# Kernel tuning notes

Measured on AMD Instinct MI355X. Metric: run time of the kernel, lower is better.

Reference implementation:

```python
import jax, jax.numpy as jnp
import numpy as np

N = 100_000   # total nodes per graph batch
E = 400_000   # directed edges per graph batch
G = 1024      # number of graphs
F_IN = 90


def _lin_init(key, fan_in, fan_out):
    s = 1.0 / np.sqrt(fan_in)
    kW, kb = jax.random.split(key)
    W = jax.random.uniform(kW, (fan_in, fan_out), jnp.float32, -s, s)
    b = jax.random.uniform(kb, (fan_out,), jnp.float32, -s, s)
    return W, b


def setup_inputs() -> dict:
    key = jax.random.key(0)
    ks = jax.random.split(key, 16)
    batch = (jnp.arange(N, dtype=jnp.int32) * G // N).astype(jnp.int32)
    inp = {
        'x1': jax.random.normal(ks[0], (N, F_IN), jnp.float32),
        'edge_index1': jax.random.randint(ks[1], (2, E), 0, N, jnp.int32),
        'batch1': batch,
        'x2': jax.random.normal(ks[2], (N, F_IN), jnp.float32),
        'edge_index2': jax.random.randint(ks[3], (2, E), 0, N, jnp.int32),
        'batch2': batch,
    }
    W1, b1 = _lin_init(ks[4], 90, 128)
    W2, b2 = _lin_init(ks[5], 128, 256)
    W3, b3 = _lin_init(ks[6], 256, 256)
    W4, b4 = _lin_init(ks[7], 256, 256)
    fc1_W, fc1_b = _lin_init(ks[8], 1024, 512)
    fc2_W, fc2_b = _lin_init(ks[9], 512, 256)
    fc3_W, fc3_b = _lin_init(ks[10], 256, 1)
    inp.update(W1=W1, b1=b1, W2=W2, b2=b2, W3=W3, b3=b3, W4=W4, b4=b4,
               fc1_W=fc1_W, fc1_b=fc1_b, fc2_W=fc2_W, fc2_b=fc2_b,
               fc3_W=fc3_W, fc3_b=fc3_b)
    return inp


def _gcn(x, W, b, src, dst, dinv):
    # GCNConv: D^{-1/2} (A + I) D^{-1/2} X W + b  (self-loops added)
    h = x @ W                                   # [N, F_out]
    norm = dinv[src] * dinv[dst]                # [E]
    agg = jax.ops.segment_sum(h[src] * norm[:, None], dst, num_segments=N)
    agg = agg + h * (dinv * dinv)[:, None]      # self-loop term
    return agg + b


def _drug_encoder(x, edge_index, batch, W1, b1, W2, b2, W3, b3, W4, b4):
    src, dst = edge_index[0], edge_index[1]
    # degree with self-loops (PyG gcn_norm)
    deg = jax.ops.segment_sum(jnp.ones(src.shape[0], x.dtype), dst, num_segments=N) + 1.0
    dinv = jax.lax.rsqrt(deg)
    x = jax.nn.relu(_gcn(x, W1, b1, src, dst, dinv))
    x = jax.nn.relu(_gcn(x, W2, b2, src, dst, dinv))
    x = jax.nn.relu(_gcn(x, W3, b3, src, dst, dinv))
    x = jax.nn.relu(_gcn(x, W4, b4, src, dst, dinv))
    gmax = jax.ops.segment_max(x, batch, num_segments=G)
    cnt = jax.ops.segment_sum(jnp.ones(N, x.dtype), batch, num_segments=G)
    gmean = jax.ops.segment_sum(x, batch, num_segments=G) / cnt[:, None]
    return jnp.concatenate([gmax, gmean], axis=1)   # [G, 512]


def reference(x1, edge_index1, batch1, x2, edge_index2, batch2,
              W1, b1, W2, b2, W3, b3, W4, b4,
              fc1_W, fc1_b, fc2_W, fc2_b, fc3_W, fc3_b):
    h1 = _drug_encoder(x1, edge_index1, batch1, W1, b1, W2, b2, W3, b3, W4, b4)
    h2 = _drug_encoder(x2, edge_index2, batch2, W1, b1, W2, b2, W3, b3, W4, b4)
    x = jnp.concatenate([h1 - h2, h2 - h1], axis=1)   # [G, 1024]
    x = jax.nn.relu(x @ fc1_W + fc1_b)                # dropout = identity (eval)
    x = jax.nn.relu(x @ fc2_W + fc2_b)
    x = jnp.tanh(x @ fc3_W + fc3_b)
    return x                                          # [G, 1]
```

## Files before the change

kernel.cpp:

```cpp
#include <hip/hip_runtime.h>
#include <hip/hip_bf16.h>

#define NN 100000
#define EE 400000
#define GG 1024

typedef _Float16 half_t;
typedef _Float16 f16x8 __attribute__((ext_vector_type(8)));
typedef float f32x4 __attribute__((ext_vector_type(4)));
typedef float f32x2 __attribute__((ext_vector_type(2)));

#define GLOAD_LDS(g, l) \
    __builtin_amdgcn_global_load_lds((const __attribute__((address_space(1))) void*)(g), \
                                     (__attribute__((address_space(3))) void*)(l), 16, 0, 0)


__global__ void k_count2(const int* __restrict__ ei1, const int* __restrict__ ei2,
                         int* __restrict__ deg) {
    int e = blockIdx.x * 256 + threadIdx.x;
    if (e >= 2 * EE) return;
    int enc = e >= EE;
    const int* ei = enc ? ei2 : ei1;
    int le = e - enc * EE;
    atomicAdd(&deg[enc * NN + ei[EE + le]], 1);
}

__global__ void k_scan_bsum(const int* __restrict__ deg, int* __restrict__ bsum, int total) {
    __shared__ int lds[256];
    int t = threadIdx.x;
    int base = blockIdx.x * 1024 + t * 4;
    int s = 0;
#pragma unroll
    for (int i = 0; i < 4; ++i) { int idx = base + i; s += (idx < total) ? deg[idx] : 0; }
    lds[t] = s;
    __syncthreads();
    for (int off = 128; off > 0; off >>= 1) {
        if (t < off) lds[t] += lds[t + off];
        __syncthreads();
    }
    if (t == 0) bsum[blockIdx.x] = lds[0];
}

__global__ void k_scan_write(const int* __restrict__ deg, const int* __restrict__ bsum,
                             int* __restrict__ rowptr, float* __restrict__ dinv,
                             int total, int totedge) {
    __shared__ int lds[256];
    __shared__ int blockoff;
    int t = threadIdx.x;
    if (t == 0) {
        int off = 0;
        for (int b = 0; b < (int)blockIdx.x; ++b) off += bsum[b];
        blockoff = off;
    }
    int base = blockIdx.x * 1024 + t * 4;
    int v[4]; int ts = 0;
#pragma unroll
    for (int i = 0; i < 4; ++i) { int idx = base + i; v[i] = (idx < total) ? deg[idx] : 0; ts += v[i]; }
    lds[t] = ts;
    __syncthreads();
    for (int off = 1; off < 256; off <<= 1) {
        int x = (t >= off) ? lds[t - off] : 0;
        __syncthreads();
        lds[t] += x;
        __syncthreads();
    }
    int excl = lds[t] - ts + blockoff;
#pragma unroll
    for (int i = 0; i < 4; ++i) {
        int idx = base + i;
        if (idx < total) {
            rowptr[idx] = excl;
            dinv[idx] = rsqrtf((float)v[i] + 1.0f);
        }
        excl += v[i];
    }
    if (blockIdx.x == 0 && t == 0) rowptr[total] = totedge;
}

__global__ void k_fill2(const int* __restrict__ ei1, const int* __restrict__ ei2,
                        const int* __restrict__ rowptr, int* __restrict__ cnt,
                        int* __restrict__ colv) {
    int e = blockIdx.x * 256 + threadIdx.x;
    if (e >= 2 * EE) return;
    int enc = e >= EE;
    const int* ei = enc ? ei2 : ei1;
    int le = e - enc * EE;
    int s = ei[le], d = ei[EE + le];
    int gd = enc * NN + d;
    int pos = rowptr[gd] + atomicAdd(&cnt[gd], 1);
    colv[pos] = s;
}

__global__ void k_starts2(const int* __restrict__ b1, const int* __restrict__ b2,
                          int* __restrict__ gstart) {
    int i = blockIdx.x * 256 + threadIdx.x;
    if (i >= 2 * NN) return;
    int enc = i >= NN;
    int il = i - enc * NN;
    const int* bat = enc ? b2 : b1;
    int* gs = gstart + enc * (GG + 1);
    int b = bat[il];
    if (il == 0) {
        for (int g = 0; g <= b; ++g) gs[g] = 0;
    } else {
        int pb = bat[il - 1];
        for (int g = pb + 1; g <= b; ++g) gs[g] = il;
    }
    if (il == NN - 1) {
        for (int g = b + 1; g <= GG; ++g) gs[g] = NN;
    }
}


__global__ void k_agg90(const float* __restrict__ x, const float* __restrict__ dinv,
                        const int* __restrict__ rowptr, const int* __restrict__ col,
                        half_t* __restrict__ out) {
    int wave = threadIdx.x >> 6;
    int lane = threadIdx.x & 63;
    int n = blockIdx.x * 4 + wave;
    if (n >= NN) return;
    bool al = lane < 45;
    float dn = dinv[n];
    f32x2 acc = {0.f, 0.f};
    if (al) acc = dn * ((const f32x2*)(x + (size_t)n * 90))[lane];
    int j0 = rowptr[n], j1 = rowptr[n + 1];
    int j = j0;
    for (; j + 4 <= j1; j += 4) {
        int s0 = col[j], s1 = col[j + 1], s2 = col[j + 2], s3 = col[j + 3];
        float d0 = dinv[s0], d1 = dinv[s1], d2 = dinv[s2], d3 = dinv[s3];
        if (al) {
            f32x2 v0 = ((const f32x2*)(x + (size_t)s0 * 90))[lane];
            f32x2 v1 = ((const f32x2*)(x + (size_t)s1 * 90))[lane];
            f32x2 v2 = ((const f32x2*)(x + (size_t)s2 * 90))[lane];
            f32x2 v3 = ((const f32x2*)(x + (size_t)s3 * 90))[lane];
            acc += d0 * v0;
            acc += d1 * v1;
            acc += d2 * v2;
            acc += d3 * v3;
        }
    }
    for (; j < j1; ++j) {
        int s = col[j];
        float ds = dinv[s];
        if (al) acc += ds * ((const f32x2*)(x + (size_t)s * 90))[lane];
    }
    float v0 = al ? dn * acc[0] : 0.f;
    float v1 = al ? dn * acc[1] : 0.f;
    half_t h0 = (half_t)v0, l0 = (half_t)(v0 - (float)h0);
    half_t h1 = (half_t)v1, l1 = (half_t)(v1 - (float)h1);
    half_t* o = out + (size_t)n * 256;
    o[2 * lane] = h0;
    o[2 * lane + 1] = h1;
    o[128 + 2 * lane] = l0;
    o[128 + 2 * lane + 1] = l1;
}

template <int VW>
__global__ void k_agg_splitv(const float* __restrict__ x, const float* __restrict__ dinv,
                             const int* __restrict__ rowptr, const int* __restrict__ col,
                             half_t* __restrict__ out) {
    constexpr int F = 64 * VW;
    typedef float fvec __attribute__((ext_vector_type(VW)));
    int wave = threadIdx.x >> 6;
    int lane = threadIdx.x & 63;
    int n = blockIdx.x * 4 + wave;
    if (n >= NN) return;
    float dn = dinv[n];
    fvec acc = dn * ((const fvec*)(x + (size_t)n * F))[lane];
    int j0 = rowptr[n], j1 = rowptr[n + 1];
    int j = j0;
    for (; j + 4 <= j1; j += 4) {
        int s0 = col[j], s1 = col[j + 1], s2 = col[j + 2], s3 = col[j + 3];
        float d0 = dinv[s0], d1 = dinv[s1], d2 = dinv[s2], d3 = dinv[s3];
        fvec v0 = ((const fvec*)(x + (size_t)s0 * F))[lane];
        fvec v1 = ((const fvec*)(x + (size_t)s1 * F))[lane];
        fvec v2 = ((const fvec*)(x + (size_t)s2 * F))[lane];
        fvec v3 = ((const fvec*)(x + (size_t)s3 * F))[lane];
        acc += d0 * v0;
        acc += d1 * v1;
        acc += d2 * v2;
        acc += d3 * v3;
    }
    for (; j < j1; ++j) {
        int s = col[j];
        acc += dinv[s] * ((const fvec*)(x + (size_t)s * F))[lane];
    }
    half_t* o = out + (size_t)n * (2 * F);
    half_t hv[VW], lv[VW];
#pragma unroll
    for (int i = 0; i < VW; ++i) {
        float v = dn * acc[i];
        hv[i] = (half_t)v;
        lv[i] = (half_t)(v - (float)hv[i]);
    }
#pragma unroll
    for (int i = 0; i < VW; ++i) o[lane * VW + i] = hv[i];
#pragma unroll
    for (int i = 0; i < VW; ++i) o[F + lane * VW + i] = lv[i];
}


__global__ void k_wprep(const float* __restrict__ W, half_t* __restrict__ Bt,
                        int K, int Kpad, int Nc) {
    int t = blockIdx.x * 256 + threadIdx.x;
    if (t >= Nc * Kpad) return;
    int n = t / Kpad, kp = t % Kpad;
    half_t h = (half_t)0.f, l = (half_t)0.f;
    if (kp < K) {
        float w = W[(size_t)kp * Nc + n];
        h = (half_t)w;
        l = (half_t)(w - (float)h);
    }
    half_t* o = Bt + (size_t)n * 3 * Kpad;
    o[kp] = h;
    o[Kpad + kp] = h;
    o[2 * Kpad + kp] = l;
}


__global__ void k_split(const float* __restrict__ in, half_t* __restrict__ out, int K) {
    int t = blockIdx.x * 256 + threadIdx.x;
    int row = t / K, k = t % K;
    float v = in[t];
    half_t h = (half_t)v;
    half_t l = (half_t)(v - (float)h);
    half_t* o = out + (size_t)row * 2 * K;
    o[k] = h;
    o[K + k] = l;
}


template <bool RELU>
__global__ __launch_bounds__(256, 2)
void k_mgemm(const half_t* __restrict__ Ap, const half_t* __restrict__ Bt,
             const float* __restrict__ bias, float* __restrict__ C,
             int M, int Kpad, int Nc) {
    __shared__ half_t As[128 * 64];
    __shared__ half_t Bs[128 * 64];
    const int tid = threadIdx.x;
    const int wave = tid >> 6, lane = tid & 63;
    const int wm = wave >> 1, wn = wave & 1;
    const int bm = blockIdx.x * 128, bn = blockIdx.y * 128;
    const int KA = 2 * Kpad, KB = 3 * Kpad;
    const int nkt = KB >> 6;
    const int aTiles = KA >> 6;

    f32x4 acc[4][4] = {};

    const int srow = tid >> 3;
    const int ch = tid & 7;

    for (int kt = 0; kt < nkt; ++kt) {
        int ka0 = ((kt < aTiles) ? kt : (kt - aTiles)) << 6;
        int kb0 = kt << 6;
        __syncthreads();
#pragma unroll
        for (int i = 0; i < 4; ++i) {
            int rl = i * 32 + srow;
            int sch = ch ^ (rl & 7);
            int gr = bm + rl; if (gr >= M) gr = M - 1;
            const half_t* ga = Ap + (size_t)gr * KA + ka0 + sch * 8;
            GLOAD_LDS(ga, (char*)As + i * 4096 + wave * 1024);
        }
#pragma unroll
        for (int i = 0; i < 4; ++i) {
            int rl = i * 32 + srow;
            int sch = ch ^ (rl & 7);
            const half_t* gb = Bt + (size_t)(bn + rl) * KB + kb0 + sch * 8;
            GLOAD_LDS(gb, (char*)Bs + i * 4096 + wave * 1024);
        }
        __syncthreads();
#pragma unroll
        for (int s = 0; s < 2; ++s) {
            f16x8 af[4], bf[4];
#pragma unroll
            for (int i = 0; i < 4; ++i) {
                int row = wm * 64 + i * 16 + (lane & 15);
                int c = s * 4 + (lane >> 4);
                af[i] = *(const f16x8*)&As[row * 64 + ((c ^ (row & 7)) << 3)];
            }
#pragma unroll
            for (int j = 0; j < 4; ++j) {
                int row = wn * 64 + j * 16 + (lane & 15);
                int c = s * 4 + (lane >> 4);
                bf[j] = *(const f16x8*)&Bs[row * 64 + ((c ^ (row & 7)) << 3)];
            }
#pragma unroll
            for (int i = 0; i < 4; ++i)
#pragma unroll
                for (int j = 0; j < 4; ++j)
                    acc[i][j] = __builtin_amdgcn_mfma_f32_16x16x32_f16(af[i], bf[j], acc[i][j], 0, 0, 0);
        }
    }

#pragma unroll
    for (int i = 0; i < 4; ++i) {
#pragma unroll
        for (int j = 0; j < 4; ++j) {
            int cc = bn + wn * 64 + j * 16 + (lane & 15);
            float bv = bias[cc];
            int r0 = bm + wm * 64 + i * 16 + (lane >> 4) * 4;
#pragma unroll
            for (int q = 0; q < 4; ++q) {
                int gr = r0 + q;
                if (gr < M) {
                    float v = acc[i][j][q] + bv;
                    if (RELU) v = fmaxf(v, 0.f);
                    C[(size_t)gr * Nc + cc] = v;
                }
            }
        }
    }
}


__global__ void k_pool(const float* __restrict__ act, const int* __restrict__ gstart,
                       float* __restrict__ h) {
    int g = blockIdx.x;
    int f = threadIdx.x;
    int s = gstart[g], e = gstart[g + 1];
    float mx = 0.f, sm = 0.f;
    for (int i = s; i < e; ++i) {
        float v = act[(size_t)i * 256 + f];
        mx = fmaxf(mx, v);
        sm += v;
    }
    float cnt = (float)(e - s);
    h[(size_t)g * 512 + f] = mx;
    h[(size_t)g * 512 + 256 + f] = (cnt > 0.f) ? sm / cnt : 0.f;
}


__global__ void k_headin_split(const float* __restrict__ h, half_t* __restrict__ xh) {
    int t = blockIdx.x * blockDim.x + threadIdx.x;
    if (t >= GG * 1024) return;
    int g = t >> 10, j = t & 1023;
    const float* h1 = h + (size_t)g * 512;
    const float* h2 = h + (size_t)(GG + g) * 512;
    float v = (j < 512) ? (h1[j] - h2[j]) : (h2[j - 512] - h1[j - 512]);
    half_t hi = (half_t)v;
    half_t lo = (half_t)(v - (float)hi);
    half_t* o = xh + (size_t)g * 2048;
    o[j] = hi;
    o[1024 + j] = lo;
}

__global__ void k_fc3(const float* __restrict__ A, const float* __restrict__ W,
                      const float* __restrict__ b, float* __restrict__ out) {
    int g = blockIdx.x * 4 + (threadIdx.x >> 6);
    int lane = threadIdx.x & 63;
    const float* a = A + (size_t)g * 256;
    float p = a[lane] * W[lane] + a[lane + 64] * W[lane + 64]
            + a[lane + 128] * W[lane + 128] + a[lane + 192] * W[lane + 192];
    for (int off = 32; off > 0; off >>= 1) p += __shfl_down(p, off);
    if (lane == 0) out[g] = tanhf(p + b[0]);
}


extern "C" void kernel_launch(void* const* d_in, const int* in_sizes, int n_in,
                              void* d_out, int out_size, void* d_ws, size_t ws_size,
                              hipStream_t stream) {
    const float* x1  = (const float*)d_in[0];
    const int*   ei1 = (const int*)d_in[1];
    const int*   ba1 = (const int*)d_in[2];
    const float* x2  = (const float*)d_in[3];
    const int*   ei2 = (const int*)d_in[4];
    const int*   ba2 = (const int*)d_in[5];
    const float* W1 = (const float*)d_in[6];
    const float* b1 = (const float*)d_in[7];
    const float* W2 = (const float*)d_in[8];
    const float* b2 = (const float*)d_in[9];
    const float* W3 = (const float*)d_in[10];
    const float* b3 = (const float*)d_in[11];
    const float* W4 = (const float*)d_in[12];
    const float* b4 = (const float*)d_in[13];
    const float* fc1W = (const float*)d_in[14];
    const float* fc1b = (const float*)d_in[15];
    const float* fc2W = (const float*)d_in[16];
    const float* fc2b = (const float*)d_in[17];
    const float* fc3W = (const float*)d_in[18];
    const float* fc3b = (const float*)d_in[19];
    float* out = (float*)d_out;

    char* ws = (char*)d_ws;
    size_t off = 0;
    auto alloc = [&](size_t bytes) -> void* {
        void* p = (void*)(ws + off);
        off += (bytes + 255) & ~(size_t)255;
        return p;
    };
    int*    dc     = (int*)alloc((size_t)4 * NN * sizeof(int));
    int*    rowptr = (int*)alloc((size_t)(2 * NN + 1) * sizeof(int));
    int*    colv   = (int*)alloc((size_t)2 * EE * sizeof(int));
    int*    bsum   = (int*)alloc(256 * sizeof(int));
    int*    gstart = (int*)alloc((size_t)2 * (GG + 1) * sizeof(int));
    float*  dinv   = (float*)alloc((size_t)2 * NN * sizeof(float));
    half_t* Ap     = (half_t*)alloc((size_t)NN * 512 * sizeof(half_t));
    float*  act    = (float*)alloc((size_t)NN * 256 * sizeof(float));
    half_t* Bt1    = (half_t*)alloc((size_t)128 * 384 * sizeof(half_t));
    half_t* Bt2    = (half_t*)alloc((size_t)256 * 384 * sizeof(half_t));
    half_t* Bt3    = (half_t*)alloc((size_t)256 * 768 * sizeof(half_t));
    half_t* Bt4    = (half_t*)alloc((size_t)256 * 768 * sizeof(half_t));
    half_t* Btf1   = (half_t*)alloc((size_t)512 * 3072 * sizeof(half_t));
    half_t* Btf2   = (half_t*)alloc((size_t)256 * 1536 * sizeof(half_t));
    float*  hpool  = (float*)alloc((size_t)2 * GG * 512 * sizeof(float));
    half_t* xhs    = (half_t*)alloc((size_t)GG * 2048 * sizeof(half_t));
    float*  t1     = (float*)alloc((size_t)GG * 512 * sizeof(float));
    half_t* t1s    = (half_t*)alloc((size_t)GG * 1024 * sizeof(half_t));
    float*  t2     = (float*)alloc((size_t)GG * 256 * sizeof(float));

    int* deg = dc;
    int* cnt = dc + 2 * NN;

    int nsb2 = (2 * NN + 1023) / 1024;
    int mt = (NN + 127) / 128;

    k_wprep<<<(128 * 128 + 255) / 256, 256, 0, stream>>>(W1, Bt1, 90, 128, 128);
    k_wprep<<<(256 * 128 + 255) / 256, 256, 0, stream>>>(W2, Bt2, 128, 128, 256);
    k_wprep<<<(256 * 256 + 255) / 256, 256, 0, stream>>>(W3, Bt3, 256, 256, 256);
    k_wprep<<<(256 * 256 + 255) / 256, 256, 0, stream>>>(W4, Bt4, 256, 256, 256);
    k_wprep<<<(512 * 1024 + 255) / 256, 256, 0, stream>>>(fc1W, Btf1, 1024, 1024, 512);
    k_wprep<<<(256 * 512 + 255) / 256, 256, 0, stream>>>(fc2W, Btf2, 512, 512, 256);

    hipMemsetAsync(dc, 0, (size_t)4 * NN * sizeof(int), stream);
    k_count2<<<(2 * EE + 255) / 256, 256, 0, stream>>>(ei1, ei2, deg);
    k_scan_bsum<<<nsb2, 256, 0, stream>>>(deg, bsum, 2 * NN);
    k_scan_write<<<nsb2, 256, 0, stream>>>(deg, bsum, rowptr, dinv, 2 * NN, 2 * EE);
    k_fill2<<<(2 * EE + 255) / 256, 256, 0, stream>>>(ei1, ei2, rowptr, cnt, colv);
    k_starts2<<<(2 * NN + 255) / 256, 256, 0, stream>>>(ba1, ba2, gstart);

    for (int p = 0; p < 2; ++p) {
        const float* x    = p ? x2 : x1;
        const int*   rp   = rowptr + p * NN;
        const float* dv   = dinv + p * NN;
        const int*   gs   = gstart + p * (GG + 1);

        k_agg90<<<(NN + 3) / 4, 256, 0, stream>>>(x, dv, rp, colv, Ap);
        k_mgemm<true><<<dim3(mt, 1), 256, 0, stream>>>(Ap, Bt1, b1, act, NN, 128, 128);
        k_agg_splitv<2><<<(NN + 3) / 4, 256, 0, stream>>>(act, dv, rp, colv, Ap);
        k_mgemm<true><<<dim3(mt, 2), 256, 0, stream>>>(Ap, Bt2, b2, act, NN, 128, 256);
        k_agg_splitv<4><<<(NN + 3) / 4, 256, 0, stream>>>(act, dv, rp, colv, Ap);
        k_mgemm<true><<<dim3(mt, 2), 256, 0, stream>>>(Ap, Bt3, b3, act, NN, 256, 256);
        k_agg_splitv<4><<<(NN + 3) / 4, 256, 0, stream>>>(act, dv, rp, colv, Ap);
        k_mgemm<true><<<dim3(mt, 2), 256, 0, stream>>>(Ap, Bt4, b4, act, NN, 256, 256);

        k_pool<<<GG, 256, 0, stream>>>(act, gs, hpool + (size_t)p * GG * 512);
    }

    k_headin_split<<<(GG * 1024 + 255) / 256, 256, 0, stream>>>(hpool, xhs);
    k_mgemm<true><<<dim3(GG / 128, 4), 256, 0, stream>>>(xhs, Btf1, fc1b, t1, GG, 1024, 512);
    k_split<<<(GG * 512 + 255) / 256, 256, 0, stream>>>(t1, t1s, 512);
    k_mgemm<true><<<dim3(GG / 128, 2), 256, 0, stream>>>(t1s, Btf2, fc2b, t2, GG, 512, 256);
    k_fc3<<<GG / 4, 256, 0, stream>>>(t2, fc3W, fc3b, out);
}
```

Measured before the change: 1.351 ms.

## Interleave both encoders by fusing one encoder's GEMM with the other's aggregation

```diff
diff --git a/kernel.cpp b/kernel.cpp
--- a/kernel.cpp
+++ b/kernel.cpp
@@ -112,12 +112,14 @@
 }
 
 
-__global__ void k_agg90(const float* __restrict__ x, const float* __restrict__ dinv,
-                        const int* __restrict__ rowptr, const int* __restrict__ col,
-                        half_t* __restrict__ out) {
+__device__ __forceinline__ void dev_agg90(int blk, const float* __restrict__ x,
+                                          const float* __restrict__ dinv,
+                                          const int* __restrict__ rowptr,
+                                          const int* __restrict__ col,
+                                          half_t* __restrict__ out) {
     int wave = threadIdx.x >> 6;
     int lane = threadIdx.x & 63;
-    int n = blockIdx.x * 4 + wave;
+    int n = blk * 4 + wave;
     if (n >= NN) return;
     bool al = lane < 45;
     float dn = dinv[n];
@@ -133,10 +135,7 @@
             f32x2 v1 = ((const f32x2*)(x + (size_t)s1 * 90))[lane];
             f32x2 v2 = ((const f32x2*)(x + (size_t)s2 * 90))[lane];
             f32x2 v3 = ((const f32x2*)(x + (size_t)s3 * 90))[lane];
-            acc += d0 * v0;
-            acc += d1 * v1;
-            acc += d2 * v2;
-            acc += d3 * v3;
+            acc += d0 * v0; acc += d1 * v1; acc += d2 * v2; acc += d3 * v3;
         }
     }
     for (; j < j1; ++j) {
@@ -156,14 +155,16 @@
 }
 
 template <int VW>
-__global__ void k_agg_splitv(const float* __restrict__ x, const float* __restrict__ dinv,
-                             const int* __restrict__ rowptr, const int* __restrict__ col,
-                             half_t* __restrict__ out) {
+__device__ __forceinline__ void dev_aggv(int blk, const float* __restrict__ x,
+                                         const float* __restrict__ dinv,
+                                         const int* __restrict__ rowptr,
+                                         const int* __restrict__ col,
+                                         half_t* __restrict__ out) {
     constexpr int F = 64 * VW;
     typedef float fvec __attribute__((ext_vector_type(VW)));
     int wave = threadIdx.x >> 6;
     int lane = threadIdx.x & 63;
-    int n = blockIdx.x * 4 + wave;
+    int n = blk * 4 + wave;
     if (n >= NN) return;
     float dn = dinv[n];
     fvec acc = dn * ((const fvec*)(x + (size_t)n * F))[lane];
@@ -176,10 +177,7 @@
         fvec v1 = ((const fvec*)(x + (size_t)s1 * F))[lane];
         fvec v2 = ((const fvec*)(x + (size_t)s2 * F))[lane];
         fvec v3 = ((const fvec*)(x + (size_t)s3 * F))[lane];
-        acc += d0 * v0;
-        acc += d1 * v1;
-        acc += d2 * v2;
-        acc += d3 * v3;
+        acc += d0 * v0; acc += d1 * v1; acc += d2 * v2; acc += d3 * v3;
     }
     for (; j < j1; ++j) {
         int s = col[j];
@@ -197,6 +195,133 @@
     for (int i = 0; i < VW; ++i) o[lane * VW + i] = hv[i];
 #pragma unroll
     for (int i = 0; i < VW; ++i) o[F + lane * VW + i] = lv[i];
+}
+
+
+template <bool RELU>
+__device__ __forceinline__ void dev_gemm(int bx, int by,
+    const half_t* __restrict__ Ap, const half_t* __restrict__ Bt,
+    const float* __restrict__ bias, float* __restrict__ C,
+    int M, int Kpad, int Nc) {
+    __shared__ half_t As[128 * 64];
+    __shared__ half_t Bs[128 * 64];
+    const int tid = threadIdx.x;
+    const int wave = tid >> 6, lane = tid & 63;
+    const int wm = wave >> 1, wn = wave & 1;
+    const int bm = bx * 128, bn = by * 128;
+    const int KA = 2 * Kpad, KB = 3 * Kpad;
+    const int nkt = KB >> 6;
+    const int aTiles = KA >> 6;
+
+    f32x4 acc[4][4] = {};
+
+    const int srow = tid >> 3;
+    const int ch = tid & 7;
+
+    for (int kt = 0; kt < nkt; ++kt) {
+        int ka0 = ((kt < aTiles) ? kt : (kt - aTiles)) << 6;
+        int kb0 = kt << 6;
+        __syncthreads();
+#pragma unroll
+        for (int i = 0; i < 4; ++i) {
+            int rl = i * 32 + srow;
+            int sch = ch ^ (rl & 7);
+            int gr = bm + rl; if (gr >= M) gr = M - 1;
+            const half_t* ga = Ap + (size_t)gr * KA + ka0 + sch * 8;
+            GLOAD_LDS(ga, (char*)As + i * 4096 + wave * 1024);
+        }
+#pragma unroll
+        for (int i = 0; i < 4; ++i) {
+            int rl = i * 32 + srow;
+            int sch = ch ^ (rl & 7);
+            const half_t* gb = Bt + (size_t)(bn + rl) * KB + kb0 + sch * 8;
+            GLOAD_LDS(gb, (char*)Bs + i * 4096 + wave * 1024);
+        }
+        __syncthreads();
+#pragma unroll
+        for (int s = 0; s < 2; ++s) {
+            f16x8 af[4], bf[4];
+#pragma unroll
+            for (int i = 0; i < 4; ++i) {
+                int row = wm * 64 + i * 16 + (lane & 15);
+                int c = s * 4 + (lane >> 4);
+                af[i] = *(const f16x8*)&As[row * 64 + ((c ^ (row & 7)) << 3)];
+            }
+#pragma unroll
+            for (int j = 0; j < 4; ++j) {
+                int row = wn * 64 + j * 16 + (lane & 15);
+                int c = s * 4 + (lane >> 4);
+                bf[j] = *(const f16x8*)&Bs[row * 64 + ((c ^ (row & 7)) << 3)];
+            }
+#pragma unroll
+            for (int i = 0; i < 4; ++i)
+#pragma unroll
+                for (int j = 0; j < 4; ++j)
+                    acc[i][j] = __builtin_amdgcn_mfma_f32_16x16x32_f16(af[i], bf[j], acc[i][j], 0, 0, 0);
+        }
+    }
+
+#pragma unroll
+    for (int i = 0; i < 4; ++i) {
+#pragma unroll
+        for (int j = 0; j < 4; ++j) {
+            int cc = bn + wn * 64 + j * 16 + (lane & 15);
+            float bv = bias[cc];
+            int r0 = bm + wm * 64 + i * 16 + (lane >> 4) * 4;
+#pragma unroll
+            for (int q = 0; q < 4; ++q) {
+                int gr = r0 + q;
+                if (gr < M) {
+                    float v = acc[i][j][q] + bv;
+                    if (RELU) v = fmaxf(v, 0.f);
+                    C[(size_t)gr * Nc + cc] = v;
+                }
+            }
+        }
+    }
+}
+
+
+__global__ void k_agg90(const float* __restrict__ x, const float* __restrict__ dinv,
+                        const int* __restrict__ rowptr, const int* __restrict__ col,
+                        half_t* __restrict__ out) {
+    dev_agg90(blockIdx.x, x, dinv, rowptr, col, out);
+}
+
+template <int VW>
+__global__ void k_agg_splitv(const float* __restrict__ x, const float* __restrict__ dinv,
+                             const int* __restrict__ rowptr, const int* __restrict__ col,
+                             half_t* __restrict__ out) {
+    dev_aggv<VW>(blockIdx.x, x, dinv, rowptr, col, out);
+}
+
+template <bool RELU>
+__global__ __launch_bounds__(256, 2)
+void k_mgemm(const half_t* __restrict__ Ap, const half_t* __restrict__ Bt,
+             const float* __restrict__ bias, float* __restrict__ C,
+             int M, int Kpad, int Nc) {
+    dev_gemm<RELU>(blockIdx.x, blockIdx.y, Ap, Bt, bias, C, M, Kpad, Nc);
+}
+
+
+template <int AGGV>
+__global__ __launch_bounds__(256, 2)
+void k_fused(int stride, int gemmBlocks, int mt,
+             const half_t* __restrict__ Ap, const half_t* __restrict__ Bt,
+             const float* __restrict__ bias, float* __restrict__ C,
+             int M, int Kpad, int Nc,
+             const float* __restrict__ xa, const float* __restrict__ dva,
+             const int* __restrict__ rpa, const int* __restrict__ cola,
+             half_t* __restrict__ outa) {
+    int q = blockIdx.x / stride, r = blockIdx.x - q * stride;
+    if (r == 0 && q < gemmBlocks) {
+        dev_gemm<true>(q % mt, q / mt, Ap, Bt, bias, C, M, Kpad, Nc);
+    } else {
+        int before = (q < gemmBlocks) ? (q + (r > 0 ? 1 : 0)) : gemmBlocks;
+        int aggIdx = blockIdx.x - before;
+        if constexpr (AGGV == 90) dev_agg90(aggIdx, xa, dva, rpa, cola, outa);
+        else dev_aggv<AGGV>(aggIdx, xa, dva, rpa, cola, outa);
+    }
 }
 
 
@@ -217,7 +342,6 @@
     o[2 * Kpad + kp] = l;
 }
 
-
 __global__ void k_split(const float* __restrict__ in, half_t* __restrict__ out, int K) {
     int t = blockIdx.x * 256 + threadIdx.x;
     int row = t / K, k = t % K;
@@ -227,90 +351,6 @@
     half_t* o = out + (size_t)row * 2 * K;
     o[k] = h;
     o[K + k] = l;
-}
-
-
-template <bool RELU>
-__global__ __launch_bounds__(256, 2)
-void k_mgemm(const half_t* __restrict__ Ap, const half_t* __restrict__ Bt,
-             const float* __restrict__ bias, float* __restrict__ C,
-             int M, int Kpad, int Nc) {
-    __shared__ half_t As[128 * 64];
-    __shared__ half_t Bs[128 * 64];
-    const int tid = threadIdx.x;
-    const int wave = tid >> 6, lane = tid & 63;
-    const int wm = wave >> 1, wn = wave & 1;
-    const int bm = blockIdx.x * 128, bn = blockIdx.y * 128;
-    const int KA = 2 * Kpad, KB = 3 * Kpad;
-    const int nkt = KB >> 6;
-    const int aTiles = KA >> 6;
-
-    f32x4 acc[4][4] = {};
-
-    const int srow = tid >> 3;
-    const int ch = tid & 7;
-
-    for (int kt = 0; kt < nkt; ++kt) {
-        int ka0 = ((kt < aTiles) ? kt : (kt - aTiles)) << 6;
-        int kb0 = kt << 6;
-        __syncthreads();
-#pragma unroll
-        for (int i = 0; i < 4; ++i) {
-            int rl = i * 32 + srow;
-            int sch = ch ^ (rl & 7);
-            int gr = bm + rl; if (gr >= M) gr = M - 1;
-            const half_t* ga = Ap + (size_t)gr * KA + ka0 + sch * 8;
-            GLOAD_LDS(ga, (char*)As + i * 4096 + wave * 1024);
-        }
-#pragma unroll
-        for (int i = 0; i < 4; ++i) {
-            int rl = i * 32 + srow;
-            int sch = ch ^ (rl & 7);
-            const half_t* gb = Bt + (size_t)(bn + rl) * KB + kb0 + sch * 8;
-            GLOAD_LDS(gb, (char*)Bs + i * 4096 + wave * 1024);
-        }
-        __syncthreads();
-#pragma unroll
-        for (int s = 0; s < 2; ++s) {
-            f16x8 af[4], bf[4];
-#pragma unroll
-            for (int i = 0; i < 4; ++i) {
-                int row = wm * 64 + i * 16 + (lane & 15);
-                int c = s * 4 + (lane >> 4);
-                af[i] = *(const f16x8*)&As[row * 64 + ((c ^ (row & 7)) << 3)];
-            }
-#pragma unroll
-            for (int j = 0; j < 4; ++j) {
-                int row = wn * 64 + j * 16 + (lane & 15);
-                int c = s * 4 + (lane >> 4);
-                bf[j] = *(const f16x8*)&Bs[row * 64 + ((c ^ (row & 7)) << 3)];
-            }
-#pragma unroll
-            for (int i = 0; i < 4; ++i)
-#pragma unroll
-                for (int j = 0; j < 4; ++j)
-                    acc[i][j] = __builtin_amdgcn_mfma_f32_16x16x32_f16(af[i], bf[j], acc[i][j], 0, 0, 0);
-        }
-    }
-
-#pragma unroll
-    for (int i = 0; i < 4; ++i) {
-#pragma unroll
-        for (int j = 0; j < 4; ++j) {
-            int cc = bn + wn * 64 + j * 16 + (lane & 15);
-            float bv = bias[cc];
-            int r0 = bm + wm * 64 + i * 16 + (lane >> 4) * 4;
-#pragma unroll
-            for (int q = 0; q < 4; ++q) {
-                int gr = r0 + q;
-                if (gr < M) {
-                    float v = acc[i][j][q] + bv;
-                    if (RELU) v = fmaxf(v, 0.f);
-                    C[(size_t)gr * Nc + cc] = v;
-                }
-            }
-        }
-    }
 }
 
 
@@ -328,6 +368,26 @@
     float cnt = (float)(e - s);
     h[(size_t)g * 512 + f] = mx;
     h[(size_t)g * 512 + 256 + f] = (cnt > 0.f) ? sm / cnt : 0.f;
+}
+
+__global__ void k_pool2(const float* __restrict__ a1, const float* __restrict__ a2,
+                        const int* __restrict__ gstart, float* __restrict__ h) {
+    int enc = blockIdx.x >> 10;
+    int g = blockIdx.x & 1023;
+    const float* act = enc ? a2 : a1;
+    const int* gs = gstart + enc * (GG + 1);
+    int f = threadIdx.x;
+    int s = gs[g], e = gs[g + 1];
+    float mx = 0.f, sm = 0.f;
+    for (int i = s; i < e; ++i) {
+        float v = act[(size_t)i * 256 + f];
+        mx = fmaxf(mx, v);
+        sm += v;
+    }
+    float cnt = (float)(e - s);
+    float* o = h + (size_t)enc * GG * 512;
+    o[(size_t)g * 512 + f] = mx;
+    o[(size_t)g * 512 + 256 + f] = (cnt > 0.f) ? sm / cnt : 0.f;
 }
 
 
@@ -382,6 +442,8 @@
     const float* fc3b = (const float*)d_in[19];
     float* out = (float*)d_out;
 
+    const bool pipe = ws_size >= (size_t)435000000ull;
+
     char* ws = (char*)d_ws;
     size_t off = 0;
     auto alloc = [&](size_t bytes) -> void* {
@@ -395,8 +457,10 @@
     int*    bsum   = (int*)alloc(256 * sizeof(int));
     int*    gstart = (int*)alloc((size_t)2 * (GG + 1) * sizeof(int));
     float*  dinv   = (float*)alloc((size_t)2 * NN * sizeof(float));
-    half_t* Ap     = (half_t*)alloc((size_t)NN * 512 * sizeof(half_t));
-    float*  act    = (float*)alloc((size_t)NN * 256 * sizeof(float));
+    half_t* Ap1    = (half_t*)alloc((size_t)NN * 512 * sizeof(half_t));
+    float*  act1   = (float*)alloc((size_t)NN * 256 * sizeof(float));
+    half_t* Ap2    = pipe ? (half_t*)alloc((size_t)NN * 512 * sizeof(half_t)) : Ap1;
+    float*  act2   = pipe ? (float*)alloc((size_t)NN * 256 * sizeof(float)) : act1;
     half_t* Bt1    = (half_t*)alloc((size_t)128 * 384 * sizeof(half_t));
     half_t* Bt2    = (half_t*)alloc((size_t)256 * 384 * sizeof(half_t));
     half_t* Bt3    = (half_t*)alloc((size_t)256 * 768 * sizeof(half_t));
@@ -414,6 +478,7 @@
 
     int nsb2 = (2 * NN + 1023) / 1024;
     int mt = (NN + 127) / 128;
+    int aggB = (NN + 3) / 4;
 
     k_wprep<<<(128 * 128 + 255) / 256, 256, 0, stream>>>(W1, Bt1, 90, 128, 128);
     k_wprep<<<(256 * 128 + 255) / 256, 256, 0, stream>>>(W2, Bt2, 128, 128, 256);
@@ -429,22 +494,50 @@
     k_fill2<<<(2 * EE + 255) / 256, 256, 0, stream>>>(ei1, ei2, rowptr, cnt, colv);
     k_starts2<<<(2 * NN + 255) / 256, 256, 0, stream>>>(ba1, ba2, gstart);
 
-    for (int p = 0; p < 2; ++p) {
-        const float* x    = p ? x2 : x1;
-        const int*   rp   = rowptr + p * NN;
-        const float* dv   = dinv + p * NN;
-        const int*   gs   = gstart + p * (GG + 1);
-
-        k_agg90<<<(NN + 3) / 4, 256, 0, stream>>>(x, dv, rp, colv, Ap);
-        k_mgemm<true><<<dim3(mt, 1), 256, 0, stream>>>(Ap, Bt1, b1, act, NN, 128, 128);
-        k_agg_splitv<2><<<(NN + 3) / 4, 256, 0, stream>>>(act, dv, rp, colv, Ap);
-        k_mgemm<true><<<dim3(mt, 2), 256, 0, stream>>>(Ap, Bt2, b2, act, NN, 128, 256);
-        k_agg_splitv<4><<<(NN + 3) / 4, 256, 0, stream>>>(act, dv, rp, colv, Ap);
-        k_mgemm<true><<<dim3(mt, 2), 256, 0, stream>>>(Ap, Bt3, b3, act, NN, 256, 256);
-        k_agg_splitv<4><<<(NN + 3) / 4, 256, 0, stream>>>(act, dv, rp, colv, Ap);
-        k_mgemm<true><<<dim3(mt, 2), 256, 0, stream>>>(Ap, Bt4, b4, act, NN, 256, 256);
-
-        k_pool<<<GG, 256, 0, stream>>>(act, gs, hpool + (size_t)p * GG * 512);
+    const int*   rp1 = rowptr;          const int*   rp2 = rowptr + NN;
+    const float* dv1 = dinv;            const float* dv2 = dinv + NN;
+
+    if (pipe) {
+        auto FUSED = [&](auto aggvTag, const half_t* Ap, const half_t* Bt, const float* bias,
+                         float* C, int Kpad, int Nc,
+                         const float* xa, const float* dva, const int* rpa, half_t* outa) {
+            constexpr int AGGV = decltype(aggvTag)::value;
+            int gB = mt * (Nc / 128);
+            int total = aggB + gB;
+            int stride = total / gB;
+            k_fused<AGGV><<<total, 256, 0, stream>>>(stride, gB, mt, Ap, Bt, bias, C,
+                                                     NN, Kpad, Nc, xa, dva, rpa, colv, outa);
+        };
+        using I90 = std::integral_constant<int, 90>;
+        using I2  = std::integral_constant<int, 2>;
+        using I4  = std::integral_constant<int, 4>;
+
+        k_agg90<<<aggB, 256, 0, stream>>>(x1, dv1, rp1, colv, Ap1);
+        FUSED(I90{}, Ap1, Bt1, b1, act1, 128, 128, x2,   dv2, rp2, Ap2);
+        FUSED(I2{},  Ap2, Bt1, b1, act2, 128, 128, act1, dv1, rp1, Ap1);
+        FUSED(I2{},  Ap1, Bt2, b2, act1, 128, 256, act2, dv2, rp2, Ap2);
+        FUSED(I4{},  Ap2, Bt2, b2, act2, 128, 256, act1, dv1, rp1, Ap1);
+        FUSED(I4{},  Ap1, Bt3, b3, act1, 256, 256, act2, dv2, rp2, Ap2);
+        FUSED(I4{},  Ap2, Bt3, b3, act2, 256, 256, act1, dv1, rp1, Ap1);
+        FUSED(I4{},  Ap1, Bt4, b4, act1, 256, 256, act2, dv2, rp2, Ap2);
+        k_mgemm<true><<<dim3(mt, 2), 256, 0, stream>>>(Ap2, Bt4, b4, act2, NN, 256, 256);
+        k_pool2<<<2 * GG, 256, 0, stream>>>(act1, act2, gstart, hpool);
+    } else {
+        for (int p = 0; p < 2; ++p) {
+            const float* x  = p ? x2 : x1;
+            const int*   rp = p ? rp2 : rp1;
+            const float* dv = p ? dv2 : dv1;
+            const int*   gs = gstart + p * (GG + 1);
+            k_agg90<<<aggB, 256, 0, stream>>>(x, dv, rp, colv, Ap1);
+            k_mgemm<true><<<dim3(mt, 1), 256, 0, stream>>>(Ap1, Bt1, b1, act1, NN, 128, 128);
+            k_agg_splitv<2><<<aggB, 256, 0, stream>>>(act1, dv, rp, colv, Ap1);
+            k_mgemm<true><<<dim3(mt, 2), 256, 0, stream>>>(Ap1, Bt2, b2, act1, NN, 128, 256);
+            k_agg_splitv<4><<<aggB, 256, 0, stream>>>(act1, dv, rp, colv, Ap1);
+            k_mgemm<true><<<dim3(mt, 2), 256, 0, stream>>>(Ap1, Bt3, b3, act1, NN, 256, 256);
+            k_agg_splitv<4><<<aggB, 256, 0, stream>>>(act1, dv, rp, colv, Ap1);
+            k_mgemm<true><<<dim3(mt, 2), 256, 0, stream>>>(Ap1, Bt4, b4, act1, NN, 256, 256);
+            k_pool<<<GG, 256, 0, stream>>>(act1, gs, hpool + (size_t)p * GG * 512);
+        }
     }
 
     k_headin_split<<<(GG * 1024 + 255) / 256, 256, 0, stream>>>(hpool, xhs);
```

Result: no change. 1.353 ms (+0.2%).

## Pack two nodes per wave in aggregation and use full-width 256-column GEMM tiles

Applied to the files above, without the earlier changes.

```diff
diff --git a/kernel.cpp b/kernel.cpp
--- a/kernel.cpp
+++ b/kernel.cpp
@@ -133,10 +133,7 @@
             f32x2 v1 = ((const f32x2*)(x + (size_t)s1 * 90))[lane];
             f32x2 v2 = ((const f32x2*)(x + (size_t)s2 * 90))[lane];
             f32x2 v3 = ((const f32x2*)(x + (size_t)s3 * 90))[lane];
-            acc += d0 * v0;
-            acc += d1 * v1;
-            acc += d2 * v2;
-            acc += d3 * v3;
+            acc += d0 * v0; acc += d1 * v1; acc += d2 * v2; acc += d3 * v3;
         }
     }
     for (; j < j1; ++j) {
@@ -156,47 +153,60 @@
 }
 
 template <int VW>
-__global__ void k_agg_splitv(const float* __restrict__ x, const float* __restrict__ dinv,
-                             const int* __restrict__ rowptr, const int* __restrict__ col,
-                             half_t* __restrict__ out) {
-    constexpr int F = 64 * VW;
+__global__ void k_aggpair(const float* __restrict__ x, const float* __restrict__ dinv,
+                          const int* __restrict__ rowptr, const int* __restrict__ col,
+                          half_t* __restrict__ out) {
+    constexpr int F = 32 * VW;
     typedef float fvec __attribute__((ext_vector_type(VW)));
     int wave = threadIdx.x >> 6;
     int lane = threadIdx.x & 63;
-    int n = blockIdx.x * 4 + wave;
-    if (n >= NN) return;
+    int sub = lane & 31;
+    int n = blockIdx.x * 8 + wave * 2 + (lane >> 5);
     float dn = dinv[n];
-    fvec acc = dn * ((const fvec*)(x + (size_t)n * F))[lane];
-    int j0 = rowptr[n], j1 = rowptr[n + 1];
-    int j = j0;
-    for (; j + 4 <= j1; j += 4) {
-        int s0 = col[j], s1 = col[j + 1], s2 = col[j + 2], s3 = col[j + 3];
-        float d0 = dinv[s0], d1 = dinv[s1], d2 = dinv[s2], d3 = dinv[s3];
-        fvec v0 = ((const fvec*)(x + (size_t)s0 * F))[lane];
-        fvec v1 = ((const fvec*)(x + (size_t)s1 * F))[lane];
-        fvec v2 = ((const fvec*)(x + (size_t)s2 * F))[lane];
-        fvec v3 = ((const fvec*)(x + (size_t)s3 * F))[lane];
-        acc += d0 * v0;
-        acc += d1 * v1;
-        acc += d2 * v2;
-        acc += d3 * v3;
-    }
-    for (; j < j1; ++j) {
-        int s = col[j];
-        acc += dinv[s] * ((const fvec*)(x + (size_t)s * F))[lane];
+    fvec acc = dn * ((const fvec*)(x + (size_t)n * F))[sub];
+    int j0 = rowptr[n];
+    int deg = rowptr[n + 1] - j0;
+    int m = max(deg, __shfl_xor(deg, 32));
+    int t = 0;
+    for (; t + 4 <= m; t += 4) {
+        bool o0 = t < deg, o1 = t + 1 < deg, o2 = t + 2 < deg, o3 = t + 3 < deg;
+        int s0 = o0 ? col[j0 + t]     : n;
+        int s1 = o1 ? col[j0 + t + 1] : n;
+        int s2 = o2 ? col[j0 + t + 2] : n;
+        int s3 = o3 ? col[j0 + t + 3] : n;
+        float w0 = o0 ? dinv[s0] : 0.f;
+        float w1 = o1 ? dinv[s1] : 0.f;
+        float w2 = o2 ? dinv[s2] : 0.f;
+        float w3 = o3 ? dinv[s3] : 0.f;
+        fvec v0 = ((const fvec*)(x + (size_t)s0 * F))[sub];
+        fvec v1 = ((const fvec*)(x + (size_t)s1 * F))[sub];
+        fvec v2 = ((const fvec*)(x + (size_t)s2 * F))[sub];
+        fvec v3 = ((const fvec*)(x + (size_t)s3 * F))[sub];
+        acc += w0 * v0; acc += w1 * v1; acc += w2 * v2; acc += w3 * v3;
+    }
+    if (t < m) {
+        bool o0 = t < deg, o1 = t + 1 < deg, o2 = t + 2 < deg;
+        bool m1 = t + 1 < m, m2 = t + 2 < m;
+        int s0 = o0 ? col[j0 + t]     : n;
+        int s1 = o1 ? col[j0 + t + 1] : n;
+        int s2 = o2 ? col[j0 + t + 2] : n;
+        float w0 = o0 ? dinv[s0] : 0.f;
+        float w1 = o1 ? dinv[s1] : 0.f;
+        float w2 = o2 ? dinv[s2] : 0.f;
+        fvec v0 = ((const fvec*)(x + (size_t)s0 * F))[sub];
+        acc += w0 * v0;
+        if (m1) { fvec v1 = ((const fvec*)(x + (size_t)s1 * F))[sub]; acc += w1 * v1; }
+        if (m2) { fvec v2 = ((const fvec*)(x + (size_t)s2 * F))[sub]; acc += w2 * v2; }
     }
     half_t* o = out + (size_t)n * (2 * F);
-    half_t hv[VW], lv[VW];
 #pragma unroll
     for (int i = 0; i < VW; ++i) {
         float v = dn * acc[i];
-        hv[i] = (half_t)v;
-        lv[i] = (half_t)(v - (float)hv[i]);
-    }
-#pragma unroll
-    for (int i = 0; i < VW; ++i) o[lane * VW + i] = hv[i];
-#pragma unroll
-    for (int i = 0; i < VW; ++i) o[F + lane * VW + i] = lv[i];
+        half_t h = (half_t)v;
+        half_t l = (half_t)(v - (float)h);
+        o[sub * VW + i] = h;
+        o[F + sub * VW + i] = l;
+    }
 }
 
 
@@ -216,7 +226,6 @@
     o[Kpad + kp] = h;
     o[2 * Kpad + kp] = l;
 }
-
 
 __global__ void k_split(const float* __restrict__ in, half_t* __restrict__ out, int K) {
     int t = blockIdx.x * 256 + threadIdx.x;
@@ -307,6 +316,90 @@
                     float v = acc[i][j][q] + bv;
                     if (RELU) v = fmaxf(v, 0.f);
                     C[(size_t)gr * Nc + cc] = v;
+                }
+            }
+        }
+    }
+}
+
+
+template <bool RELU>
+__global__ __launch_bounds__(256, 2)
+void k_mgemm256(const half_t* __restrict__ Ap, const half_t* __restrict__ Bt,
+                const float* __restrict__ bias, float* __restrict__ C,
+                int M, int Kpad) {
+    __shared__ half_t As[128 * 64];
+    __shared__ half_t Bs[256 * 64];
+    const int tid = threadIdx.x;
+    const int wave = tid >> 6, lane = tid & 63;
+    const int wm = wave >> 1, wn = wave & 1;
+    const int bm = blockIdx.x * 128;
+    const int KA = 2 * Kpad, KB = 3 * Kpad;
+    const int nkt = KB >> 6;
+    const int aTiles = KA >> 6;
+
+    f32x4 acc[4][8] = {};
+
+    const int srow = tid >> 3;
+    const int ch = tid & 7;
+
+    for (int kt = 0; kt < nkt; ++kt) {
+        int ka0 = ((kt < aTiles) ? kt : (kt - aTiles)) << 6;
+        int kb0 = kt << 6;
+        __syncthreads();
+#pragma unroll
+        for (int i = 0; i < 4; ++i) {
+            int rl = i * 32 + srow;
+            int sch = ch ^ (rl & 7);
+            int gr = bm + rl; if (gr >= M) gr = M - 1;
+            const half_t* ga = Ap + (size_t)gr * KA + ka0 + sch * 8;
+            GLOAD_LDS(ga, (char*)As + i * 4096 + wave * 1024);
+        }
+#pragma unroll
+        for (int i = 0; i < 8; ++i) {
+            int rl = i * 32 + srow;
+            int sch = ch ^ (rl & 7);
+            const half_t* gb = Bt + (size_t)rl * KB + kb0 + sch * 8;
+            GLOAD_LDS(gb, (char*)Bs + i * 4096 + wave * 1024);
+        }
+        __syncthreads();
+#pragma unroll
+        for (int s = 0; s < 2; ++s) {
+            f16x8 af[4], bf[8];
+#pragma unroll
+            for (int i = 0; i < 4; ++i) {
+                int row = wm * 64 + i * 16 + (lane & 15);
+                int c = s * 4 + (lane >> 4);
+                af[i] = *(const f16x8*)&As[row * 64 + ((c ^ (row & 7)) << 3)];
+            }
+#pragma unroll
+            for (int j = 0; j < 8; ++j) {
+                int row = wn * 128 + j * 16 + (lane & 15);
+                int c = s * 4 + (lane >> 4);
+                bf[j] = *(const f16x8*)&Bs[row * 64 + ((c ^ (row & 7)) << 3)];
+            }
+#pragma unroll
+            for (int i = 0; i < 4; ++i)
+#pragma unroll
+                for (int j = 0; j < 8; ++j)
+                    acc[i][j] = __builtin_amdgcn_mfma_f32_16x16x32_f16(af[i], bf[j], acc[i][j], 0, 0, 0);
+        }
+    }
+
+#pragma unroll
+    for (int i = 0; i < 4; ++i) {
+#pragma unroll
+        for (int j = 0; j < 8; ++j) {
+            int cc = wn * 128 + j * 16 + (lane & 15);
+            float bv = bias[cc];
+            int r0 = bm + wm * 64 + i * 16 + (lane >> 4) * 4;
+#pragma unroll
+            for (int q = 0; q < 4; ++q) {
+                int gr = r0 + q;
+                if (gr < M) {
+                    float v = acc[i][j][q] + bv;
+                    if (RELU) v = fmaxf(v, 0.f);
+                    C[(size_t)gr * 256 + cc] = v;
                 }
             }
         }
@@ -430,19 +523,19 @@
     k_starts2<<<(2 * NN + 255) / 256, 256, 0, stream>>>(ba1, ba2, gstart);
 
     for (int p = 0; p < 2; ++p) {
-        const float* x    = p ? x2 : x1;
-        const int*   rp   = rowptr + p * NN;
-        const float* dv   = dinv + p * NN;
-        const int*   gs   = gstart + p * (GG + 1);
+        const float* x  = p ? x2 : x1;
+        const int*   rp = rowptr + p * NN;
+        const float* dv = dinv + p * NN;
+        const int*   gs = gstart + p * (GG + 1);
 
         k_agg90<<<(NN + 3) / 4, 256, 0, stream>>>(x, dv, rp, colv, Ap);
         k_mgemm<true><<<dim3(mt, 1), 256, 0, stream>>>(Ap, Bt1, b1, act, NN, 128, 128);
-        k_agg_splitv<2><<<(NN + 3) / 4, 256, 0, stream>>>(act, dv, rp, colv, Ap);
-        k_mgemm<true><<<dim3(mt, 2), 256, 0, stream>>>(Ap, Bt2, b2, act, NN, 128, 256);
-        k_agg_splitv<4><<<(NN + 3) / 4, 256, 0, stream>>>(act, dv, rp, colv, Ap);
-        k_mgemm<true><<<dim3(mt, 2), 256, 0, stream>>>(Ap, Bt3, b3, act, NN, 256, 256);
-        k_agg_splitv<4><<<(NN + 3) / 4, 256, 0, stream>>>(act, dv, rp, colv, Ap);
-        k_mgemm<true><<<dim3(mt, 2), 256, 0, stream>>>(Ap, Bt4, b4, act, NN, 256, 256);
+        k_aggpair<4><<<NN / 8, 256, 0, stream>>>(act, dv, rp, colv, Ap);
+        k_mgemm256<true><<<mt, 256, 0, stream>>>(Ap, Bt2, b2, act, NN, 128);
+        k_aggpair<8><<<NN / 8, 256, 0, stream>>>(act, dv, rp, colv, Ap);
+        k_mgemm256<true><<<mt, 256, 0, stream>>>(Ap, Bt3, b3, act, NN, 256);
+        k_aggpair<8><<<NN / 8, 256, 0, stream>>>(act, dv, rp, colv, Ap);
+        k_mgemm256<true><<<mt, 256, 0, stream>>>(Ap, Bt4, b4, act, NN, 256);
 
         k_pool<<<GG, 256, 0, stream>>>(act, gs, hpool + (size_t)p * GG * 512);
     }
```

Measured after the change: 1.376 ms. Within noise of the previous version (+1.8%).
